# Performance work log

Measured on AMD Instinct MI355X. Metric: run time of the kernel, lower is better.

The kernel has to match this reference:

```python
import jax, jax.numpy as jnp
import numpy as np
from jax import lax

B, ROWS, COLS, K, LATENT = 8, 1536, 16, 32, 16
EPS_REG = 0.01  # torchsort regularization_strength
BIG = 1e30


def setup_inputs() -> dict:
    key = jax.random.key(0)
    ks = jax.random.split(key, 12)
    def w(k, shape):
        return (jax.random.normal(k, shape, jnp.float32) / np.sqrt(shape[0])).astype(jnp.float32)
    return {
        "table": jax.random.uniform(ks[0], (B, ROWS, COLS), jnp.float32),
        "enc_w1": w(ks[1], (COLS, 32)), "enc_b1": 0.01 * jax.random.normal(ks[2], (32,), jnp.float32),
        "enc_w2": w(ks[3], (32, 64)),   "enc_b2": 0.01 * jax.random.normal(ks[4], (64,), jnp.float32),
        "mean_w": w(ks[5], (64, LATENT)), "mean_b": 0.01 * jax.random.normal(ks[6], (LATENT,), jnp.float32),
        "dec_w1": w(ks[7], (LATENT, 32)), "dec_b1": 0.01 * jax.random.normal(ks[8], (32,), jnp.float32),
        "dec_w2": w(ks[9], (32, COLS)),   "dec_b2": 0.01 * jax.random.normal(ks[10], (COLS,), jnp.float32),
        "labels": jax.random.randint(ks[11], (ROWS,), 0, K, jnp.int32),
        "BlockSize": 64,
        "current_epoch": 0,
        "baseline": 0,
    }


def _soft_rank_l2(s, eps):
    # Exact soft_rank (Blondel et al. / torchsort, l2 reg, ascending):
    # project s/eps onto permutahedron of (n,...,1).
    n = s.shape[0]
    x = s / eps
    perm = jnp.argsort(-x)            # descending sort
    xs = x[perm]
    w = jnp.arange(n, 0, -1, dtype=x.dtype)
    # dual = non-increasing isotonic fit of y = xs - w == -iso_inc(-(xs - w))
    y = -(xs - w)
    S = jnp.concatenate([jnp.zeros((1,), x.dtype), jnp.cumsum(y)])
    idx = jnp.arange(n)
    length = jnp.maximum(idx[None, :] - idx[:, None] + 1, 1).astype(x.dtype)
    A = (S[1:][None, :] - S[:n][:, None]) / length           # mean(y[j..k])  [j,k]
    A = jnp.where(idx[None, :] >= idx[:, None], A, BIG)
    Bm = lax.cummin(A, axis=1, reverse=True)                  # min_{k>=i} A[j,k]
    Cm = lax.cummax(Bm, axis=0)                               # max_{j<=i} ...
    iso_inc = jnp.diagonal(Cm)
    dual = -iso_inc
    primal = xs - dual
    inv = jnp.argsort(perm)
    return primal[inv]


def _forward(table, enc_w1, enc_b1, enc_w2, enc_b2, mean_w, mean_b,
             dec_w1, dec_b1, dec_w2, dec_b2, labels, BlockSize):
    b = table.shape[0]
    # VAE (autoencoder path; z = latent mean)
    h = jax.nn.relu(table @ enc_w1 + enc_b1)
    h = jax.nn.relu(h @ enc_w2 + enc_b2)
    z = h @ mean_w + mean_b                                   # [B, rows, 16]
    r = jax.nn.relu(z @ dec_w1 + dec_b1)
    recon = jax.nn.relu(r @ dec_w2 + dec_b2)
    loss = jnp.mean((recon - table) ** 2)
    # clustering scores (labels fixed from batch 0, shared across batch)
    onehot = jax.nn.one_hot(labels, K, dtype=z.dtype)         # [rows, K]
    counts = jnp.maximum(onehot.sum(0), 1.0)                  # [K]
    centers = jnp.einsum('brd,rk->bkd', z, onehot) / counts[None, :, None]
    center_data = centers[:, labels, :]                       # gather back [B, rows, 16]
    d2 = jnp.mean((z - center_data) ** 2, axis=-1)            # [B, rows]
    mn = d2.min(axis=1, keepdims=True); mx = d2.max(axis=1, keepdims=True)
    d2 = (d2 - mn) / (mx - mn)
    scores = d2 + labels.astype(z.dtype)[None, :]
    # training branch
    smn = scores.min(axis=1, keepdims=True); smx = scores.max(axis=1, keepdims=True)
    scaled = (scores - smn) / (smx - smn) * jnp.asarray(b, z.dtype)  # * len(table)
    ranks = jax.vmap(lambda s: _soft_rank_l2(s, EPS_REG))(scaled)
    rank_idx = jnp.argsort(jnp.argsort(scores, axis=1), axis=1) // BlockSize + 1
    rows = table.shape[1]
    return (ranks.reshape(b, rows, 1), rank_idx.reshape(b, rows, 1),
            scores.reshape(b, rows, 1), loss)


def reference(table, enc_w1, enc_b1, enc_w2, enc_b2, mean_w, mean_b,
              dec_w1, dec_b1, dec_w2, dec_b2, labels, BlockSize,
              current_epoch, baseline):
    return _forward(table, enc_w1, enc_b1, enc_w2, enc_b2, mean_w, mean_b,
                    dec_w1, dec_b1, dec_w2, dec_b2, labels, BlockSize)
```

## Files before the change

kernel.cpp:

```cpp
#include <hip/hip_runtime.h>

#define BATCH 8
#define ROWS 1536
#define KCLS 32
#define NTOT (BATCH*ROWS)
#define ELEMS (NTOT*16)
#define SSTRIDE 3073
#define BIGF 1.0e30f

enum : int {
  WS_Z     = 0,
  WS_XS    = WS_Z + NTOT*16,
  WS_S     = WS_XS + NTOT,
  WS_DESC  = WS_S + BATCH*SSTRIDE,
  WS_ASCP  = WS_DESC + NTOT,
  WS_DSCP  = WS_ASCP + 4*NTOT,
  WS_GPART = WS_DSCP + 4*NTOT,
  WS_LOSSP = WS_GPART + BATCH*96*512,
  WS_D2    = WS_LOSSP + 768,
  WS_MM    = WS_D2 + NTOT,
  WS_CPAR2 = WS_MM + 96,
  WS_CNT   = WS_CPAR2 + BATCH*8*512,
};
#define WS_CPART WS_GPART

#define LW1  0
#define LB1  512
#define LW2  544
#define LB2  2592
#define LMW  2656
#define LMB  3680
#define LDW1 3696
#define LDB1 4208
#define LDW2 4240
#define LDB2 4752
#define LTOT 4768

#define AX   0
#define AH1  16
#define AH2  48
#define AZ   112
#define AR1  128
#define AREC 144
#define ASTRIDE 164

#define RPB 16

template<int IN_BASE, int IN_N, int OUT_BASE, int OUT_PW, int OUT_TOT,
         int WOFF, int BOFF, bool RELU>
__device__ __forceinline__ void layerw(float* __restrict__ act,
                                       const float* __restrict__ wsh,
                                       int lrow, int fway)
{
  const int o0 = fway * OUT_PW;
  float acc[OUT_PW];
#pragma unroll
  for (int j = 0; j < OUT_PW; ++j) acc[j] = wsh[BOFF + o0 + j];

  const float4* arow = reinterpret_cast<const float4*>(&act[lrow*ASTRIDE + IN_BASE]);
#pragma unroll 2
  for (int i4 = 0; i4 < IN_N/4; ++i4) {
    float4 sv = arow[i4];
    float svx[4];
    svx[0] = sv.x; svx[1] = sv.y; svx[2] = sv.z; svx[3] = sv.w;
#pragma unroll
    for (int u = 0; u < 4; ++u) {
      const float s = svx[u];
      const float* wp = &wsh[WOFF + (i4*4 + u)*OUT_TOT + o0];
      if constexpr (OUT_PW == 1) {
        acc[0] = fmaf(s, wp[0], acc[0]);
      } else if constexpr (OUT_PW == 2) {
        float2 w = *reinterpret_cast<const float2*>(wp);
        acc[0] = fmaf(s, w.x, acc[0]);
        acc[1] = fmaf(s, w.y, acc[1]);
      } else {
#pragma unroll
        for (int q = 0; q < OUT_PW/4; ++q) {
          float4 w = reinterpret_cast<const float4*>(wp)[q];
          acc[q*4+0] = fmaf(s, w.x, acc[q*4+0]);
          acc[q*4+1] = fmaf(s, w.y, acc[q*4+1]);
          acc[q*4+2] = fmaf(s, w.z, acc[q*4+2]);
          acc[q*4+3] = fmaf(s, w.w, acc[q*4+3]);
        }
      }
    }
  }
  float* orow = &act[lrow*ASTRIDE + OUT_BASE + o0];
  if constexpr (OUT_PW == 1) {
    orow[0] = RELU ? fmaxf(acc[0], 0.f) : acc[0];
  } else if constexpr (OUT_PW == 2) {
    float2 v;
    v.x = RELU ? fmaxf(acc[0], 0.f) : acc[0];
    v.y = RELU ? fmaxf(acc[1], 0.f) : acc[1];
    *reinterpret_cast<float2*>(orow) = v;
  } else {
#pragma unroll
    for (int q = 0; q < OUT_PW/4; ++q) {
      float4 v;
      v.x = RELU ? fmaxf(acc[q*4+0], 0.f) : acc[q*4+0];
      v.y = RELU ? fmaxf(acc[q*4+1], 0.f) : acc[q*4+1];
      v.z = RELU ? fmaxf(acc[q*4+2], 0.f) : acc[q*4+2];
      v.w = RELU ? fmaxf(acc[q*4+3], 0.f) : acc[q*4+3];
      reinterpret_cast<float4*>(orow)[q] = v;
    }
  }
}

__global__ __launch_bounds__(256, 4) void k1_ae(
    const float* __restrict__ table,
    const float* __restrict__ w1, const float* __restrict__ b1,
    const float* __restrict__ w2, const float* __restrict__ b2,
    const float* __restrict__ mw, const float* __restrict__ mb,
    const float* __restrict__ dw1, const float* __restrict__ db1,
    const float* __restrict__ dw2, const float* __restrict__ db2,
    const int* __restrict__ labels,
    float* __restrict__ ws)
{
  const int tid  = threadIdx.x;
  const int lrow = tid & (RPB-1);
  const int fway = tid >> 4;
  const int blk  = blockIdx.x;
  const int b    = blk / 96;
  const int ch   = blk % 96;

  __shared__ float wsh[LTOT];
  __shared__ float act[RPB * ASTRIDE];
  __shared__ int   lbl[RPB];
  __shared__ float lred[4];

  {
    float4* d4 = reinterpret_cast<float4*>(wsh);
#define CPY(off, src, nf4) \
    { const float4* p = reinterpret_cast<const float4*>(src); \
      for (int t = tid; t < (nf4); t += 256) d4[(off)/4 + t] = p[t]; }
    CPY(LW1,  w1,  128) CPY(LB1,  b1,  8)  CPY(LW2,  w2,  512)
    CPY(LB2,  b2,  16)  CPY(LMW,  mw,  256) CPY(LMB,  mb,  4)
    CPY(LDW1, dw1, 128) CPY(LDB1, db1, 8)  CPY(LDW2, dw2, 128)
    CPY(LDB2, db2, 4)
#undef CPY
    if (tid < RPB) lbl[tid] = labels[ch * RPB + tid];
    if (tid < RPB*4) {
      const float4 v = reinterpret_cast<const float4*>(table)[blk*(RPB*4) + tid];
      reinterpret_cast<float4*>(act)[(tid >> 2)*(ASTRIDE/4) + (tid & 3)] = v;
    }
  }
  __syncthreads();

  layerw<AX,  16, AH1, 2, 32, LW1,  LB1,  true >(act, wsh, lrow, fway);
  __syncthreads();
  layerw<AH1, 32, AH2, 4, 64, LW2,  LB2,  true >(act, wsh, lrow, fway);
  __syncthreads();
  layerw<AH2, 64, AZ,  1, 16, LMW,  LMB,  false>(act, wsh, lrow, fway);
  __syncthreads();

  if (tid < RPB*4) {
    const float4 zv =
      reinterpret_cast<const float4*>(act)[(tid >> 2)*(ASTRIDE/4) + (AZ/4) + (tid & 3)];
    reinterpret_cast<float4*>(ws + WS_Z)[blk*(RPB*4) + tid] = zv;
  }

  layerw<AZ,  16, AR1, 2, 32, LDW1, LDB1, true >(act, wsh, lrow, fway);
  __syncthreads();
  layerw<AR1, 32, AREC,1, 16, LDW2, LDB2, true >(act, wsh, lrow, fway);
  __syncthreads();

  {
    const float d = act[lrow*ASTRIDE + AREC + fway] - act[lrow*ASTRIDE + AX + fway];
    float ls = d * d;
    for (int off = 32; off > 0; off >>= 1) ls += __shfl_down(ls, off);
    if ((tid & 63) == 0) lred[tid >> 6] = ls;
    __syncthreads();
    if (tid == 0) ws[WS_LOSSP + blk] = (lred[0] + lred[1]) + (lred[2] + lred[3]);
  }

  {
    float a0 = 0.f, a1 = 0.f;
    const int d0 = tid & 15, k0 = tid >> 4;
    const int k1c = k0 + 16;
#pragma unroll
    for (int rr = 0; rr < RPB; ++rr) {
      const int lb = lbl[rr];
      const float zv = act[rr*ASTRIDE + AZ + d0];
      a0 += (lb == k0)  ? zv : 0.f;
      a1 += (lb == k1c) ? zv : 0.f;
    }
    ws[WS_CPART + (b*96 + ch)*512 + tid]       = a0;
    ws[WS_CPART + (b*96 + ch)*512 + 256 + tid] = a1;
  }
}

__global__ __launch_bounds__(512) void kcen(const int* __restrict__ labels,
                                            float* __restrict__ ws,
                                            float* __restrict__ out)
{
  const int bi = blockIdx.x;
  const int b = bi >> 3, g = bi & 7;
  const int tid = threadIdx.x;

  const float* cp = ws + WS_CPART + (b*96 + g*12)*512 + tid;
  float s = 0.f;
#pragma unroll
  for (int c = 0; c < 12; ++c) s += cp[c*512];
  ws[WS_CPAR2 + (b*8 + g)*512 + tid] = s;

  if (bi == 0) {
    __shared__ int icnt[KCLS];
    __shared__ float red[512];
    if (tid < KCLS) icnt[tid] = 0;
    __syncthreads();
    atomicAdd(&icnt[labels[tid]], 1);
    atomicAdd(&icnt[labels[512 + tid]], 1);
    atomicAdd(&icnt[labels[1024 + tid]], 1);
    red[tid] = ws[WS_LOSSP + tid] + ((tid < 256) ? ws[WS_LOSSP + 512 + tid] : 0.f);
    __syncthreads();
    for (int off = 256; off > 0; off >>= 1) {
      if (tid < off) red[tid] += red[tid + off];
      __syncthreads();
    }
    if (tid == 0) out[3*NTOT] = red[0] / (float)ELEMS;
    if (tid < KCLS) reinterpret_cast<int*>(ws)[WS_CNT + tid] = icnt[tid];
  }
}

__global__ __launch_bounds__(256) void kd2(const int* __restrict__ labels,
                                           float* __restrict__ ws)
{
  const int bi = blockIdx.x;
  const int b = bi / 6, ib = bi % 6;
  const int tid = threadIdx.x;

  __shared__ float cent[512];
  __shared__ float rmn[256], rmx[256];
  __shared__ int ci[KCLS];

  if (tid < KCLS) ci[tid] = reinterpret_cast<const int*>(ws)[WS_CNT + tid];
  float s1 = 0.f, s2 = 0.f;
#pragma unroll
  for (int g = 0; g < 8; ++g) {
    s1 += ws[WS_CPAR2 + (b*8 + g)*512 + tid];
    s2 += ws[WS_CPAR2 + (b*8 + g)*512 + 256 + tid];
  }
  __syncthreads();
  {
    int cn1 = ci[tid >> 4];         cn1 = cn1 > 1 ? cn1 : 1;
    int cn2 = ci[(tid + 256) >> 4]; cn2 = cn2 > 1 ? cn2 : 1;
    cent[tid]       = s1 / (float)cn1;
    cent[tid + 256] = s2 / (float)cn2;
  }
  __syncthreads();

  const int r = ib*256 + tid;
  const int lb = labels[r];
  const float4* zp = reinterpret_cast<const float4*>(ws + WS_Z + (b*ROWS + r)*16);
  const float4* cq = reinterpret_cast<const float4*>(&cent[lb*16]);
  float s = 0.f;
#pragma unroll
  for (int q = 0; q < 4; ++q) {
    float4 zv = zp[q], cv = cq[q];
    float d0 = zv.x - cv.x, d1 = zv.y - cv.y, d2_ = zv.z - cv.z, d3 = zv.w - cv.w;
    s += d0*d0 + d1*d1 + d2_*d2_ + d3*d3;
  }
  const float dv = s / 16.f;
  ws[WS_D2 + b*ROWS + r] = dv;
  rmn[tid] = dv; rmx[tid] = dv;
  __syncthreads();
  for (int off = 128; off > 0; off >>= 1) {
    if (tid < off) {
      rmn[tid] = fminf(rmn[tid], rmn[tid + off]);
      rmx[tid] = fmaxf(rmx[tid], rmx[tid + off]);
    }
    __syncthreads();
  }
  if (tid == 0) {
    ws[WS_MM + bi*2]     = rmn[0];
    ws[WS_MM + bi*2 + 1] = rmx[0];
  }
}

__global__ __launch_bounds__(256) void kcount(const int* __restrict__ labels,
                                              float* __restrict__ ws,
                                              float* __restrict__ out)
{
  const int bi = blockIdx.x;
  const int jb = bi & 3, rb = (bi >> 2) % 6, b = bi / 24;
  const int tid = threadIdx.x;

  alignas(16) __shared__ float s_l[ROWS];

  float mn = 3.0e38f, mx = -3.0e38f;
#pragma unroll
  for (int c = 0; c < 6; ++c) {
    mn = fminf(mn, ws[WS_MM + (b*6 + c)*2]);
    mx = fmaxf(mx, ws[WS_MM + (b*6 + c)*2 + 1]);
  }

#pragma unroll
  for (int c = 0; c < 6; ++c) {
    const int r = c*256 + tid;
    const float sc = (ws[WS_D2 + b*ROWS + r] - mn) / (mx - mn) + (float)labels[r];
    s_l[r] = sc;
    if (jb == 0 && c == rb) out[2*NTOT + b*ROWS + r] = sc;
  }
  __syncthreads();

  const int r0 = rb*256 + tid;
  const float si = s_l[r0];
  int asc = 0, dsc = 0;
  const int j0 = jb*384;
  const float4* s4p = reinterpret_cast<const float4*>(&s_l[j0]);
#pragma unroll 4
  for (int kk = 0; kk < 96; ++kk) {
    const float4 s4 = s4p[kk];
    const int j = j0 + kk*4;
    const bool t0 = (s4.x == si && j   < r0);
    const bool t1 = (s4.y == si && j+1 < r0);
    const bool t2 = (s4.z == si && j+2 < r0);
    const bool t3 = (s4.w == si && j+3 < r0);
    asc += (s4.x < si || t0) ? 1 : 0;
    asc += (s4.y < si || t1) ? 1 : 0;
    asc += (s4.z < si || t2) ? 1 : 0;
    asc += (s4.w < si || t3) ? 1 : 0;
    dsc += (s4.x > si || t0) ? 1 : 0;
    dsc += (s4.y > si || t1) ? 1 : 0;
    dsc += (s4.z > si || t2) ? 1 : 0;
    dsc += (s4.w > si || t3) ? 1 : 0;
  }
  int* wsi = reinterpret_cast<int*>(ws);
  wsi[WS_ASCP + jb*NTOT + b*ROWS + r0] = asc;
  wsi[WS_DSCP + jb*NTOT + b*ROWS + r0] = dsc;
}

__global__ __launch_bounds__(256) void k67(const int* __restrict__ bsp,
                                           float* __restrict__ ws,
                                           float* __restrict__ out)
{
  const int b = blockIdx.x, tid = threadIdx.x;
  const int lane = tid & 63, wav = tid >> 6;
  __shared__ float xs_l[ROWS];
  __shared__ float rmn[256], rmx[256];
  __shared__ float wtot[4];
  const int* wsi = reinterpret_cast<const int*>(ws);
  int* wsw = reinterpret_cast<int*>(ws);
  const int BS = *bsp;

  int dscv[6];
  float sv[6];
  float tmn = 3.0e38f, tmx = -3.0e38f;
#pragma unroll
  for (int c = 0; c < 6; ++c) {
    const int r = c*256 + tid;
    const int idx = b*ROWS + r;
    int asc = 0, dsc = 0;
#pragma unroll
    for (int jb = 0; jb < 4; ++jb) {
      asc += wsi[WS_ASCP + jb*NTOT + idx];
      dsc += wsi[WS_DSCP + jb*NTOT + idx];
    }
    out[NTOT + idx] = (float)(asc / BS + 1);
    wsw[WS_DESC + idx] = dsc;
    dscv[c] = dsc;
    const float sc = out[2*NTOT + idx];
    sv[c] = sc;
    tmn = fminf(tmn, sc); tmx = fmaxf(tmx, sc);
  }
  rmn[tid] = tmn; rmx[tid] = tmx;
  __syncthreads();
  for (int off = 128; off > 0; off >>= 1) {
    if (tid < off) {
      rmn[tid] = fminf(rmn[tid], rmn[tid + off]);
      rmx[tid] = fmaxf(rmx[tid], rmx[tid + off]);
    }
    __syncthreads();
  }
  const float smn = rmn[0], smx = rmx[0];
  __syncthreads();

#pragma unroll
  for (int c = 0; c < 6; ++c) {
    const float scl = (sv[c] - smn) / (smx - smn) * 8.0f;
    xs_l[dscv[c]] = scl / 0.01f;
  }
  __syncthreads();

  const int base = tid * 6;
  float y[6], own = 0.f;
#pragma unroll
  for (int u = 0; u < 6; ++u) {
    ws[WS_XS + b*ROWS + base + u] = xs_l[base + u];
    y[u] = (float)(ROWS - (base + u)) - xs_l[base + u];
    own += y[u];
  }
  float v = own;
#pragma unroll
  for (int d = 1; d < 64; d <<= 1) {
    float o = __shfl_up(v, d);
    if (lane >= d) v += o;
  }
  if (lane == 63) wtot[wav] = v;
  __syncthreads();
  float wpre = 0.f;
  for (int w = 0; w < wav; ++w) wpre += wtot[w];
  float run = wpre + (v - own);
  float* S = ws + WS_S + b*SSTRIDE;
#pragma unroll
  for (int u = 0; u < 6; ++u) { S[base + u] = run; run += y[u]; }
  if (tid == 255) S[ROWS] = run;
#pragma unroll
  for (int u = 0; u < 6; ++u) S[ROWS + 1 + tid*6 + u] = BIGF;
}

__global__ __launch_bounds__(256) void k8a(float* __restrict__ ws)
{
  const int bi = blockIdx.x;
  const int c = bi & 7, ib = (bi >> 3) % 6, b = bi / 48;
  const int tid = threadIdx.x;
  __shared__ float Sseg[448];
  __shared__ float invl[192];
  const float* S = ws + WS_S + b*SSTRIDE;
  const int ibase = ib*256;
  const int segbase = ibase + c*192 + 1;
  Sseg[tid] = S[segbase + tid];
  if (tid < 192) {
    Sseg[256 + tid] = S[segbase + 256 + tid];
    invl[tid] = 1.0f / (float)(c*192 + tid + 1);
  }
  __syncthreads();
  const int i = ibase + tid;
  const float Si = S[i];
  float gm = 3.0e38f;
#pragma unroll 8
  for (int k = 0; k < 192; ++k)
    gm = fminf(gm, (Sseg[tid + k] - Si) * invl[k]);
  ws[WS_GPART + (b*8 + c)*ROWS + i] = gm;
}

__global__ __launch_bounds__(768) void k8b(float* __restrict__ ws,
                                           float* __restrict__ out)
{
  const int b = blockIdx.x, tid = threadIdx.x;
  const int lane = tid & 63, wav = tid >> 6;
  __shared__ float g[ROWS];
  __shared__ float wtot[12];
  for (int t = tid; t < ROWS; t += 768) {
    float gm = 3.0e38f;
#pragma unroll
    for (int c = 0; c < 8; ++c)
      gm = fminf(gm, ws[WS_GPART + (b*8 + c)*ROWS + t]);
    g[t] = gm;
  }
  __syncthreads();
  const float a = g[2*tid], cc = g[2*tid + 1];
  float v = fmaxf(a, cc);
#pragma unroll
  for (int d = 1; d < 64; d <<= 1) {
    float o = __shfl_up(v, d);
    if (lane >= d) v = fmaxf(v, o);
  }
  if (lane == 63) wtot[wav] = v;
  __syncthreads();
  float wpre = -3.0e38f;
  for (int w = 0; w < wav; ++w) wpre = fmaxf(wpre, wtot[w]);
  float lex = __shfl_up(v, 1);
  if (lane == 0) lex = -3.0e38f;
  const float excl = fmaxf(wpre, lex);
  const float i0 = fmaxf(excl, a);
  const float i1 = fmaxf(i0, cc);
  g[2*tid] = i0; g[2*tid + 1] = i1;
  __syncthreads();
  const float* xs = ws + WS_XS + b*ROWS;
  const int* desc = reinterpret_cast<const int*>(ws) + WS_DESC + b*ROWS;
  for (int t = tid; t < ROWS; t += 768) {
    const int dr = desc[t];
    out[b*ROWS + t] = xs[dr] + g[dr];
  }
}

extern "C" void kernel_launch(void* const* d_in, const int* in_sizes, int n_in,
                              void* d_out, int out_size, void* d_ws, size_t ws_size,
                              hipStream_t stream) {
  const float* table = (const float*)d_in[0];
  const float* w1  = (const float*)d_in[1];
  const float* b1  = (const float*)d_in[2];
  const float* w2  = (const float*)d_in[3];
  const float* b2  = (const float*)d_in[4];
  const float* mw  = (const float*)d_in[5];
  const float* mb  = (const float*)d_in[6];
  const float* dw1 = (const float*)d_in[7];
  const float* db1 = (const float*)d_in[8];
  const float* dw2 = (const float*)d_in[9];
  const float* db2 = (const float*)d_in[10];
  const int* labels = (const int*)d_in[11];
  const int* bsp    = (const int*)d_in[12];
  float* out = (float*)d_out;
  float* ws  = (float*)d_ws;

  k1_ae<<<768, 256, 0, stream>>>(table, w1, b1, w2, b2, mw, mb, dw1, db1, dw2, db2, labels, ws);
  kcen<<<64, 512, 0, stream>>>(labels, ws, out);
  kd2<<<48, 256, 0, stream>>>(labels, ws);
  kcount<<<192, 256, 0, stream>>>(labels, ws, out);
  k67<<<8, 256, 0, stream>>>(bsp, ws, out);
  k8a<<<384, 256, 0, stream>>>(ws);
  k8b<<<8, 768, 0, stream>>>(ws, out);
}
```

Before: 59.49 us.

## Fuse centroid reduction into distance kernel and widen rank-prep block

Merges the centroid partial-sum kernel and the distance kernel into one launch. Each block now recomputes label counts and sums all 96 centroid partials directly, and block 0 also reduces the loss. This removes a launch and an intermediate buffer but makes each block reread the full partial buffer. Separately, the rank-prep kernel moves to 1024 threads with wave-shuffle min/max reductions and a shorter per-thread scan, to add parallelism to an 8-block kernel.

Measured after the change: 65.04 us. 9.3% more time.

```diff
diff --git a/kernel.cpp b/kernel.cpp
--- a/kernel.cpp
+++ b/kernel.cpp
@@ -19,8 +19,6 @@
   WS_LOSSP = WS_GPART + BATCH*96*512,
   WS_D2    = WS_LOSSP + 768,
   WS_MM    = WS_D2 + NTOT,
-  WS_CPAR2 = WS_MM + 96,
-  WS_CNT   = WS_CPAR2 + BATCH*8*512,
 };
 #define WS_CPART WS_GPART
 
@@ -189,80 +187,62 @@
   }
 }
 
-__global__ __launch_bounds__(512) void kcen(const int* __restrict__ labels,
+__global__ __launch_bounds__(256) void kmid(const int* __restrict__ labels,
                                             float* __restrict__ ws,
                                             float* __restrict__ out)
-{
-  const int bi = blockIdx.x;
-  const int b = bi >> 3, g = bi & 7;
-  const int tid = threadIdx.x;
-
-  const float* cp = ws + WS_CPART + (b*96 + g*12)*512 + tid;
-  float s = 0.f;
-#pragma unroll
-  for (int c = 0; c < 12; ++c) s += cp[c*512];
-  ws[WS_CPAR2 + (b*8 + g)*512 + tid] = s;
-
-  if (bi == 0) {
-    __shared__ int icnt[KCLS];
-    __shared__ float red[512];
-    if (tid < KCLS) icnt[tid] = 0;
-    __syncthreads();
-    atomicAdd(&icnt[labels[tid]], 1);
-    atomicAdd(&icnt[labels[512 + tid]], 1);
-    atomicAdd(&icnt[labels[1024 + tid]], 1);
-    red[tid] = ws[WS_LOSSP + tid] + ((tid < 256) ? ws[WS_LOSSP + 512 + tid] : 0.f);
-    __syncthreads();
-    for (int off = 256; off > 0; off >>= 1) {
-      if (tid < off) red[tid] += red[tid + off];
-      __syncthreads();
-    }
-    if (tid == 0) out[3*NTOT] = red[0] / (float)ELEMS;
-    if (tid < KCLS) reinterpret_cast<int*>(ws)[WS_CNT + tid] = icnt[tid];
-  }
-}
-
-__global__ __launch_bounds__(256) void kd2(const int* __restrict__ labels,
-                                           float* __restrict__ ws)
 {
   const int bi = blockIdx.x;
   const int b = bi / 6, ib = bi % 6;
   const int tid = threadIdx.x;
 
+  __shared__ int   cnt[KCLS];
+  __shared__ int   lbls[256];
   __shared__ float cent[512];
   __shared__ float rmn[256], rmx[256];
-  __shared__ int ci[KCLS];
-
-  if (tid < KCLS) ci[tid] = reinterpret_cast<const int*>(ws)[WS_CNT + tid];
+
+  if (tid < KCLS) cnt[tid] = 0;
+  __syncthreads();
+#pragma unroll
+  for (int c = 0; c < 6; ++c) {
+    const int lb = labels[c*256 + tid];
+    if (c == ib) lbls[tid] = lb;
+    atomicAdd(&cnt[lb], 1);
+  }
+
   float s1 = 0.f, s2 = 0.f;
-#pragma unroll
-  for (int g = 0; g < 8; ++g) {
-    s1 += ws[WS_CPAR2 + (b*8 + g)*512 + tid];
-    s2 += ws[WS_CPAR2 + (b*8 + g)*512 + 256 + tid];
-  }
-  __syncthreads();
-  {
-    int cn1 = ci[tid >> 4];         cn1 = cn1 > 1 ? cn1 : 1;
-    int cn2 = ci[(tid + 256) >> 4]; cn2 = cn2 > 1 ? cn2 : 1;
+  {
+    const float* cp = ws + WS_CPART + (b*96)*512;
+#pragma unroll 8
+    for (int c = 0; c < 96; ++c) {
+      s1 += cp[c*512 + tid];
+      s2 += cp[c*512 + 256 + tid];
+    }
+  }
+  __syncthreads();
+  {
+    int cn1 = cnt[tid >> 4];         cn1 = cn1 > 1 ? cn1 : 1;
+    int cn2 = cnt[(tid + 256) >> 4]; cn2 = cn2 > 1 ? cn2 : 1;
     cent[tid]       = s1 / (float)cn1;
     cent[tid + 256] = s2 / (float)cn2;
   }
   __syncthreads();
 
   const int r = ib*256 + tid;
-  const int lb = labels[r];
-  const float4* zp = reinterpret_cast<const float4*>(ws + WS_Z + (b*ROWS + r)*16);
-  const float4* cq = reinterpret_cast<const float4*>(&cent[lb*16]);
-  float s = 0.f;
-#pragma unroll
-  for (int q = 0; q < 4; ++q) {
-    float4 zv = zp[q], cv = cq[q];
-    float d0 = zv.x - cv.x, d1 = zv.y - cv.y, d2_ = zv.z - cv.z, d3 = zv.w - cv.w;
-    s += d0*d0 + d1*d1 + d2_*d2_ + d3*d3;
-  }
-  const float dv = s / 16.f;
-  ws[WS_D2 + b*ROWS + r] = dv;
-  rmn[tid] = dv; rmx[tid] = dv;
+  {
+    const int lb = lbls[tid];
+    const float4* zp = reinterpret_cast<const float4*>(ws + WS_Z + (b*ROWS + r)*16);
+    const float4* cq = reinterpret_cast<const float4*>(&cent[lb*16]);
+    float s = 0.f;
+#pragma unroll
+    for (int q = 0; q < 4; ++q) {
+      float4 zv = zp[q], cv = cq[q];
+      float d0 = zv.x - cv.x, d1 = zv.y - cv.y, d2_ = zv.z - cv.z, d3 = zv.w - cv.w;
+      s += d0*d0 + d1*d1 + d2_*d2_ + d3*d3;
+    }
+    const float dv = s / 16.f;
+    ws[WS_D2 + b*ROWS + r] = dv;
+    rmn[tid] = dv; rmx[tid] = dv;
+  }
   __syncthreads();
   for (int off = 128; off > 0; off >>= 1) {
     if (tid < off) {
@@ -274,6 +254,17 @@
   if (tid == 0) {
     ws[WS_MM + bi*2]     = rmn[0];
     ws[WS_MM + bi*2 + 1] = rmx[0];
+  }
+
+  if (bi == 0) {
+    __syncthreads();
+    rmn[tid] = ws[WS_LOSSP + tid] + ws[WS_LOSSP + 256 + tid] + ws[WS_LOSSP + 512 + tid];
+    __syncthreads();
+    for (int off = 128; off > 0; off >>= 1) {
+      if (tid < off) rmn[tid] += rmn[tid + off];
+      __syncthreads();
+    }
+    if (tid == 0) out[3*NTOT] = rmn[0] / (float)ELEMS;
   }
 }
 
@@ -330,26 +321,23 @@
   wsi[WS_DSCP + jb*NTOT + b*ROWS + r0] = dsc;
 }
 
-__global__ __launch_bounds__(256) void k67(const int* __restrict__ bsp,
-                                           float* __restrict__ ws,
-                                           float* __restrict__ out)
+__global__ __launch_bounds__(1024) void k67(const int* __restrict__ bsp,
+                                            float* __restrict__ ws,
+                                            float* __restrict__ out)
 {
   const int b = blockIdx.x, tid = threadIdx.x;
   const int lane = tid & 63, wav = tid >> 6;
   __shared__ float xs_l[ROWS];
-  __shared__ float rmn[256], rmx[256];
-  __shared__ float wtot[4];
+  __shared__ float wr1[16], wr2[16];
+  __shared__ float wtot[16];
   const int* wsi = reinterpret_cast<const int*>(ws);
   int* wsw = reinterpret_cast<int*>(ws);
   const int BS = *bsp;
 
-  int dscv[6];
-  float sv[6];
-  float tmn = 3.0e38f, tmx = -3.0e38f;
-#pragma unroll
-  for (int c = 0; c < 6; ++c) {
-    const int r = c*256 + tid;
-    const int idx = b*ROWS + r;
+  int dsc1 = 0, dsc2 = 0;
+  float sv1, sv2 = 0.f;
+  {
+    const int idx = b*ROWS + tid;
     int asc = 0, dsc = 0;
 #pragma unroll
     for (int jb = 0; jb < 4; ++jb) {
@@ -358,37 +346,50 @@
     }
     out[NTOT + idx] = (float)(asc / BS + 1);
     wsw[WS_DESC + idx] = dsc;
-    dscv[c] = dsc;
-    const float sc = out[2*NTOT + idx];
-    sv[c] = sc;
-    tmn = fminf(tmn, sc); tmx = fmaxf(tmx, sc);
-  }
-  rmn[tid] = tmn; rmx[tid] = tmx;
-  __syncthreads();
-  for (int off = 128; off > 0; off >>= 1) {
-    if (tid < off) {
-      rmn[tid] = fminf(rmn[tid], rmn[tid + off]);
-      rmx[tid] = fmaxf(rmx[tid], rmx[tid + off]);
-    }
-    __syncthreads();
-  }
-  const float smn = rmn[0], smx = rmx[0];
-  __syncthreads();
-
-#pragma unroll
-  for (int c = 0; c < 6; ++c) {
-    const float scl = (sv[c] - smn) / (smx - smn) * 8.0f;
-    xs_l[dscv[c]] = scl / 0.01f;
-  }
-  __syncthreads();
-
-  const int base = tid * 6;
-  float y[6], own = 0.f;
-#pragma unroll
-  for (int u = 0; u < 6; ++u) {
-    ws[WS_XS + b*ROWS + base + u] = xs_l[base + u];
-    y[u] = (float)(ROWS - (base + u)) - xs_l[base + u];
-    own += y[u];
+    dsc1 = dsc;
+    sv1 = out[2*NTOT + idx];
+  }
+  if (tid < 512) {
+    const int idx = b*ROWS + 1024 + tid;
+    int asc = 0, dsc = 0;
+#pragma unroll
+    for (int jb = 0; jb < 4; ++jb) {
+      asc += wsi[WS_ASCP + jb*NTOT + idx];
+      dsc += wsi[WS_DSCP + jb*NTOT + idx];
+    }
+    out[NTOT + idx] = (float)(asc / BS + 1);
+    wsw[WS_DESC + idx] = dsc;
+    dsc2 = dsc;
+    sv2 = out[2*NTOT + idx];
+  }
+
+  {
+    float tmn = sv1, tmx = sv1;
+    if (tid < 512) { tmn = fminf(tmn, sv2); tmx = fmaxf(tmx, sv2); }
+    for (int off = 32; off > 0; off >>= 1) {
+      tmn = fminf(tmn, __shfl_down(tmn, off));
+      tmx = fmaxf(tmx, __shfl_down(tmx, off));
+    }
+    if (lane == 0) { wr1[wav] = tmn; wr2[wav] = tmx; }
+  }
+  __syncthreads();
+  float smn = 3.0e38f, smx = -3.0e38f;
+#pragma unroll
+  for (int w = 0; w < 16; ++w) {
+    smn = fminf(smn, wr1[w]); smx = fmaxf(smx, wr2[w]);
+  }
+
+  xs_l[dsc1] = (sv1 - smn) / (smx - smn) * 8.0f / 0.01f;
+  if (tid < 512) xs_l[dsc2] = (sv2 - smn) / (smx - smn) * 8.0f / 0.01f;
+  __syncthreads();
+
+  float y0 = 0.f, y1 = 0.f, own = 0.f;
+  int base = 0;
+  if (tid < 768) {
+    base = tid * 2;
+    y0 = (float)(ROWS - base)     - xs_l[base];
+    y1 = (float)(ROWS - base - 1) - xs_l[base + 1];
+    own = y0 + y1;
   }
   float v = own;
 #pragma unroll
@@ -400,13 +401,16 @@
   __syncthreads();
   float wpre = 0.f;
   for (int w = 0; w < wav; ++w) wpre += wtot[w];
-  float run = wpre + (v - own);
   float* S = ws + WS_S + b*SSTRIDE;
-#pragma unroll
-  for (int u = 0; u < 6; ++u) { S[base + u] = run; run += y[u]; }
-  if (tid == 255) S[ROWS] = run;
-#pragma unroll
-  for (int u = 0; u < 6; ++u) S[ROWS + 1 + tid*6 + u] = BIGF;
+  if (tid < 768) {
+    float run = wpre + (v - own);
+    S[base] = run; run += y0;
+    S[base + 1] = run; run += y1;
+    if (tid == 767) S[ROWS] = run;
+    ws[WS_XS + b*ROWS + base]     = xs_l[base];
+    ws[WS_XS + b*ROWS + base + 1] = xs_l[base + 1];
+  }
+  for (int p = tid; p < SSTRIDE - ROWS - 1; p += 1024) S[ROWS + 1 + p] = BIGF;
 }
 
 __global__ __launch_bounds__(256) void k8a(float* __restrict__ ws)
@@ -495,10 +499,9 @@
   float* ws  = (float*)d_ws;
 
   k1_ae<<<768, 256, 0, stream>>>(table, w1, b1, w2, b2, mw, mb, dw1, db1, dw2, db2, labels, ws);
-  kcen<<<64, 512, 0, stream>>>(labels, ws, out);
-  kd2<<<48, 256, 0, stream>>>(labels, ws);
+  kmid<<<48, 256, 0, stream>>>(labels, ws, out);
   kcount<<<192, 256, 0, stream>>>(labels, ws, out);
-  k67<<<8, 256, 0, stream>>>(bsp, ws, out);
+  k67<<<8, 1024, 0, stream>>>(bsp, ws, out);
   k8a<<<384, 256, 0, stream>>>(ws);
   k8b<<<8, 768, 0, stream>>>(ws, out);
 }
```
